# Kernel tuning notes

Measured on AMD Instinct MI355X. Metric: run time of the kernel, lower is better.

The kernel has to match this reference:

```python
import jax, jax.numpy as jnp
import numpy as np

N, E, G = 20000, 320000, 256
FXD, FXT, OD = 78, 954, 128


def _lin(key, fan_in, fan_out, scale=0.05):
    return jax.random.normal(key, (fan_in, fan_out), dtype=jnp.float32) * scale


def setup_inputs() -> dict:
    key = jax.random.key(0)
    ks = jax.random.split(key, 24)
    inp = {
        "x1": jax.random.normal(ks[0], (N, FXD), dtype=jnp.float32),
        "edge_index1": jax.random.randint(ks[1], (2, E), 0, N, dtype=jnp.int32),
        "batch1": (jnp.arange(N, dtype=jnp.int32) * G) // N,  # sorted, every graph non-empty
        "x2": jax.random.normal(ks[2], (N, FXD), dtype=jnp.float32),
        "edge_index2": jax.random.randint(ks[3], (2, E), 0, N, dtype=jnp.int32),
        "batch2": (jnp.arange(N, dtype=jnp.int32) * G) // N,
        "cell": jax.random.normal(ks[4], (G, FXT), dtype=jnp.float32),
        # GCNConv weights (shared across the two drug branches, as in the module)
        "Wc1": _lin(ks[5], FXD, FXD), "bc1": jnp.zeros((FXD,), jnp.float32),
        "Wc2": _lin(ks[6], FXD, FXD * 2), "bc2": jnp.zeros((FXD * 2,), jnp.float32),
        "Wc3": _lin(ks[7], FXD * 2, FXD * 4), "bc3": jnp.zeros((FXD * 4,), jnp.float32),
        "Wg1": _lin(ks[8], FXD * 4, FXD * 2), "bg1": jnp.zeros((FXD * 2,), jnp.float32),
        "Wg2": _lin(ks[9], FXD * 2, OD), "bg2": jnp.zeros((OD,), jnp.float32),
        # cell reduction MLP 954 -> 2048 -> 512 -> 256
        "Wr1": _lin(ks[10], FXT, 2048), "br1": jnp.zeros((2048,), jnp.float32),
        "Wr2": _lin(ks[11], 2048, 512), "br2": jnp.zeros((512,), jnp.float32),
        "Wr3": _lin(ks[12], 512, OD * 2), "br3": jnp.zeros((OD * 2,), jnp.float32),
        # head MLP 512 -> 1024 -> 512 -> 128 -> 2
        "Wf1": _lin(ks[13], OD * 4, 1024), "bf1": jnp.zeros((1024,), jnp.float32),
        "Wf2": _lin(ks[14], 1024, 512), "bf2": jnp.zeros((512,), jnp.float32),
        "Wf3": _lin(ks[15], 512, 128), "bf3": jnp.zeros((128,), jnp.float32),
        "Wo": _lin(ks[16], 128, 2), "bo": jnp.zeros((2,), jnp.float32),
    }
    return inp


def gcn_conv(x, W, b, src, dst, n):
    """PyG GCNConv: h = D^{-1/2}(A+I)D^{-1/2} (x W) + b (self-loops added)."""
    h = x @ W
    loops = jnp.arange(n, dtype=src.dtype)
    s = jnp.concatenate([src, loops])
    d = jnp.concatenate([dst, loops])
    deg = jax.ops.segment_sum(jnp.ones_like(s, dtype=h.dtype), d, num_segments=n)
    dinv = jax.lax.rsqrt(deg)  # deg >= 1 due to self-loops
    norm = dinv[s] * dinv[d]  # [E+N]
    out = jax.ops.segment_sum(h[s] * norm[:, None], d, num_segments=n)
    return out + b


def drug_branch(x, ei, batch, Wc1, bc1, Wc2, bc2, Wc3, bc3, Wg1, bg1, Wg2, bg2):
    src, dst = ei[0], ei[1]
    n = x.shape[0]
    x = jax.nn.relu(gcn_conv(x, Wc1, bc1, src, dst, n))
    x = jax.nn.relu(gcn_conv(x, Wc2, bc2, src, dst, n))
    x = jax.nn.relu(gcn_conv(x, Wc3, bc3, src, dst, n))
    x = jax.ops.segment_max(x, batch, num_segments=G)  # global max pool -> [G, 312]
    x = jax.nn.relu(x @ Wg1 + bg1)
    x = x @ Wg2 + bg2  # dropout is identity in eval mode
    return x


def reference(x1, edge_index1, batch1, x2, edge_index2, batch2, cell,
              Wc1, bc1, Wc2, bc2, Wc3, bc3, Wg1, bg1, Wg2, bg2,
              Wr1, br1, Wr2, br2, Wr3, br3,
              Wf1, bf1, Wf2, bf2, Wf3, bf3, Wo, bo):
    g1 = drug_branch(x1, edge_index1, batch1, Wc1, bc1, Wc2, bc2, Wc3, bc3, Wg1, bg1, Wg2, bg2)
    g2 = drug_branch(x2, edge_index2, batch2, Wc1, bc1, Wc2, bc2, Wc3, bc3, Wg1, bg1, Wg2, bg2)
    # F.normalize(cell, p=2, dim=1)
    cv = cell / jnp.maximum(jnp.linalg.norm(cell, axis=1, keepdims=True), 1e-12)
    cv = jax.nn.relu(cv @ Wr1 + br1)
    cv = jax.nn.relu(cv @ Wr2 + br2)
    cv = jax.nn.relu(cv @ Wr3 + br3)
    xc = jnp.concatenate([g1, g2, cv], axis=1)  # [G, 512]
    xc = jax.nn.relu(xc @ Wf1 + bf1)
    xc = jax.nn.relu(xc @ Wf2 + bf2)
    xc = jax.nn.relu(xc @ Wf3 + bf3)
    return xc @ Wo + bo  # [G, 2]
```

## Files before the change

### kernel.cpp

```cpp
#include <hip/hip_runtime.h>

#define N_NODES 20000
#define N_EDGES 320000
#define N_GRAPH 256
#define ECHUNK 2048

__device__ __forceinline__ ushort f2b(float f) {
  unsigned u = __float_as_uint(f);
  u += 0x7FFFu + ((u >> 16) & 1u);
  return (ushort)(u >> 16);
}
__device__ __forceinline__ float b2f(ushort u) {
  return __uint_as_float(((unsigned)u) << 16);
}

typedef __attribute__((ext_vector_type(8))) short bf16x8;
typedef __attribute__((ext_vector_type(4))) float f32x4;

template <int POOL>
__launch_bounds__(256)
__global__ void gemm_mfma(const ushort* __restrict__ A, int lda,
                          const ushort* __restrict__ Bt, int ldbt,
                          void* __restrict__ Cv, int ldc, int zstride,
                          const float* __restrict__ bias,
                          int Nr, int Kpad, int M, int do_relu, int obf,
                          int kchunk, int swz,
                          const int* __restrict__ bA, const int* __restrict__ bB,
                          int nsplit, int gA, int gB, int gTot) {
  constexpr int BM = 128, BN = 64, BK = 32, LK = 40;
  __shared__ __align__(16) ushort Asl[BM][LK];
  __shared__ __align__(16) ushort Bsl[BN][LK];
  const int tid = threadIdx.x;
  int bx, by;
  if (swz) {
    const int Cc = (M + BN - 1) / BN;
    const int R = (Nr + BM - 1) / BM;
    const int RR = (R + 7) >> 3;
    const int xz = blockIdx.x & 7, g = blockIdx.x >> 3;
    const int q = g / Cc;
    by = xz * RR + q;
    bx = g - q * Cc;
    if (by >= R) return;
  } else {
    bx = blockIdx.x; by = blockIdx.y;
  }
  const int row0 = by * BM, col0 = bx * BN;

  const int lane = tid & 63, w = tid >> 6;
  const int a_r = tid >> 1, a_h = tid & 1;
  const int b_r = tid >> 2, b_o = (tid & 3) * 8;

  const int klo = blockIdx.z * kchunk;
  const int khi = min(klo + kchunk, Kpad);
  const int nst = (khi - klo) / BK;

  uint4 pa0, pa1, pb0;
  auto load_tile = [&](int k0) {
    if (row0 + a_r < Nr) {
      const uint4* p = (const uint4*)(A + (size_t)(row0 + a_r) * lda + k0 + a_h * 16);
      pa0 = p[0]; pa1 = p[1];
    } else {
      pa0 = make_uint4(0u, 0u, 0u, 0u); pa1 = pa0;
    }
    pb0 = *(const uint4*)(Bt + (size_t)(col0 + b_r) * ldbt + k0 + b_o);
  };
  auto commit = [&]() {
    *(uint4*)&Asl[a_r][a_h * 16] = pa0;
    *(uint4*)&Asl[a_r][a_h * 16 + 8] = pa1;
    *(uint4*)&Bsl[b_r][b_o] = pb0;
  };

  f32x4 acc[2][4] = {};
  const int mrow = w * 32;
  const int lm = lane & 15, lq = (lane >> 4) * 8;

  load_tile(klo);
  for (int t = 0; t < nst; ++t) {
    commit();
    __syncthreads();
    if (t + 1 < nst) load_tile(klo + (t + 1) * BK);
    bf16x8 af0 = *(const bf16x8*)&Asl[mrow + lm][lq];
    bf16x8 af1 = *(const bf16x8*)&Asl[mrow + 16 + lm][lq];
    bf16x8 bf0 = *(const bf16x8*)&Bsl[lm][lq];
    bf16x8 bf1 = *(const bf16x8*)&Bsl[16 + lm][lq];
    bf16x8 bf2 = *(const bf16x8*)&Bsl[32 + lm][lq];
    bf16x8 bf3 = *(const bf16x8*)&Bsl[48 + lm][lq];
    acc[0][0] = __builtin_amdgcn_mfma_f32_16x16x32_bf16(af0, bf0, acc[0][0], 0, 0, 0);
    acc[0][1] = __builtin_amdgcn_mfma_f32_16x16x32_bf16(af0, bf1, acc[0][1], 0, 0, 0);
    acc[0][2] = __builtin_amdgcn_mfma_f32_16x16x32_bf16(af0, bf2, acc[0][2], 0, 0, 0);
    acc[0][3] = __builtin_amdgcn_mfma_f32_16x16x32_bf16(af0, bf3, acc[0][3], 0, 0, 0);
    acc[1][0] = __builtin_amdgcn_mfma_f32_16x16x32_bf16(af1, bf0, acc[1][0], 0, 0, 0);
    acc[1][1] = __builtin_amdgcn_mfma_f32_16x16x32_bf16(af1, bf1, acc[1][1], 0, 0, 0);
    acc[1][2] = __builtin_amdgcn_mfma_f32_16x16x32_bf16(af1, bf2, acc[1][2], 0, 0, 0);
    acc[1][3] = __builtin_amdgcn_mfma_f32_16x16x32_bf16(af1, bf3, acc[1][3], 0, 0, 0);
    __syncthreads();
  }

  const int rquad = (lane >> 4) * 4;

  if constexpr (POOL) {
    __shared__ int Ps[4][64];
    Ps[tid >> 6][tid & 63] = 0;
    __syncthreads();
    const int g0 = (row0 < nsplit) ? gA + bA[row0] : gB + bB[row0 - nsplit];
    int gr8[2][4];
#pragma unroll
    for (int mt = 0; mt < 2; ++mt)
#pragma unroll
      for (int r = 0; r < 4; ++r) {
        const int rr = row0 + mrow + mt * 16 + rquad + r;
        gr8[mt][r] = (rr < Nr)
                         ? ((rr < nsplit) ? gA + bA[rr] : gB + bB[rr - nsplit])
                         : -1;
      }
#pragma unroll
    for (int mt = 0; mt < 2; ++mt)
#pragma unroll
      for (int nt = 0; nt < 4; ++nt) {
        const int cl = nt * 16 + lm;
        if (col0 + cl >= M) continue;
        const float bv = bias[col0 + cl];
#pragma unroll
        for (int r = 0; r < 4; ++r) {
          const int g = gr8[mt][r];
          if (g < 0) continue;
          const float v = fmaxf(acc[mt][nt][r] + bv, 0.f);
          atomicMax(&Ps[g - g0][cl], __float_as_int(v));
        }
      }
    __syncthreads();
    const int s = tid >> 6, c = tid & 63;
    const int g = g0 + s, cc = col0 + c;
    if (g < gTot && cc < M)
      atomicMax((int*)Cv + (size_t)g * ldc + cc, Ps[s][c]);
    return;
  }

  if (zstride) {
    float* Cz = (float*)Cv + (size_t)blockIdx.z * zstride;
#pragma unroll
    for (int mt = 0; mt < 2; ++mt)
#pragma unroll
      for (int nt = 0; nt < 4; ++nt) {
        const int cc = col0 + nt * 16 + lm;
        if (cc >= M) continue;
#pragma unroll
        for (int r = 0; r < 4; ++r) {
          const int rr = row0 + mrow + mt * 16 + rquad + r;
          if (rr < Nr) Cz[(size_t)rr * ldc + cc] = acc[mt][nt][r];
        }
      }
    return;
  }
#pragma unroll
  for (int mt = 0; mt < 2; ++mt) {
#pragma unroll
    for (int nt = 0; nt < 4; ++nt) {
      const int cc = col0 + nt * 16 + lm;
      if (cc >= M) continue;
      const float bv = bias ? bias[cc] : 0.f;
#pragma unroll
      for (int r = 0; r < 4; ++r) {
        const int rr = row0 + mrow + mt * 16 + rquad + r;
        if (rr >= Nr) continue;
        float v = acc[mt][nt][r] + bv;
        if (do_relu) v = fmaxf(v, 0.f);
        if (obf) ((ushort*)Cv)[(size_t)rr * ldc + cc] = f2b(v);
        else     ((float*)Cv)[(size_t)rr * ldc + cc] = v;
      }
    }
  }
}

__global__ void wcvt_all(const float* __restrict__ W1, const float* __restrict__ W2,
                         const float* __restrict__ W3, const float* __restrict__ Wr1,
                         const float* __restrict__ Wr2, const float* __restrict__ Wf1,
                         ushort* __restrict__ T1, ushort* __restrict__ T2,
                         ushort* __restrict__ T3, ushort* __restrict__ R1,
                         ushort* __restrict__ R2, ushort* __restrict__ F1) {
  const int A1 = 128 * 96, A2 = A1 + 192 * 96, A3 = A2 + 320 * 160;
  const int S1 = 2048 * 960, S2 = 512 * 2048, S3 = 1024 * 512;
  int gid = blockIdx.x * blockDim.x + threadIdx.x;
  if (gid < A1) {
    int n = gid / 96, k = gid - n * 96;
    T1[gid] = (n < 78 && k < 78) ? f2b(W1[k * 78 + n]) : 0;
  } else if (gid < A2) {
    int g = gid - A1;
    int n = g / 96, k = g - n * 96;
    T2[g] = (n < 156 && k < 78) ? f2b(W2[k * 156 + n]) : 0;
  } else if (gid < A3) {
    int g = gid - A2;
    int n = g / 160, k = g - n * 160;
    T3[g] = (n < 312 && k < 156) ? f2b(W3[k * 312 + n]) : 0;
  } else if (gid < A3 + S1) {
    int g = gid - A3;
    int n = g / 960, k = g - n * 960;
    R1[g] = (k < 954) ? f2b(Wr1[(size_t)k * 2048 + n]) : 0;
  } else if (gid < A3 + S1 + S2) {
    int g = gid - A3 - S1;
    int n = g / 2048, k = g - n * 2048;
    R2[g] = f2b(Wr2[(size_t)k * 512 + n]);
  } else if (gid < A3 + S1 + S2 + S3) {
    int g = gid - A3 - S1 - S2;
    int n = g / 512, k = g - n * 512;
    F1[g] = f2b(Wf1[(size_t)k * 1024 + n]);
  }
}

template<int BM, int BN, int TM, int TN>
__launch_bounds__(256)
__global__ void gemm_t(const float* __restrict__ A, int lda,
                       const float* __restrict__ B, int ldb,
                       float* __restrict__ C, int ldc, int zstride,
                       const float* __restrict__ bias,
                       int Nr, int K, int M, int do_relu, int kchunk) {
  constexpr int BK = 16;
  constexpr int LDA = BM + 4;
  __shared__ __align__(16) float As[BK][LDA];
  __shared__ __align__(16) float Bs[BK][BN];
  const int tid = threadIdx.x;
  const int row0 = blockIdx.y * BM, col0 = blockIdx.x * BN;
  constexpr int NX = BN / TN;
  const int tx = tid % NX, ty = tid / NX;
  float acc[TM][TN] = {};
  const int klo = blockIdx.z * kchunk;
  const int khi = min(klo + kchunk, K);

  constexpr int AIT = BM * BK / 4 / 256;
  constexpr int BIT = BK * BN / 4 / 256;
  float4 pa[AIT], pb[BIT];

  auto load_tile = [&](int k0) {
#pragma unroll
    for (int it = 0; it < AIT; ++it) {
      const int s = it * 256 + tid;
      const int row = s >> 2, kq = (s & 3) << 2;
      float4 av = make_float4(0.f, 0.f, 0.f, 0.f);
      const int gr = row0 + row, gk = k0 + kq;
      if (gr < Nr) {
        const float* Ap = A + (size_t)gr * lda + gk;
        if (gk + 3 < khi) { av.x = Ap[0]; av.y = Ap[1]; av.z = Ap[2]; av.w = Ap[3]; }
        else {
          if (gk     < khi) av.x = Ap[0];
          if (gk + 1 < khi) av.y = Ap[1];
          if (gk + 2 < khi) av.z = Ap[2];
        }
      }
      pa[it] = av;
    }
#pragma unroll
    for (int it = 0; it < BIT; ++it) {
      const int s = it * 256 + tid;
      const int kr = s / (BN / 4), c = (s % (BN / 4)) << 2;
      float4 bv = make_float4(0.f, 0.f, 0.f, 0.f);
      const int gk = k0 + kr, gc = col0 + c;
      if (gk < khi) {
        const float* Bp = B + (size_t)gk * ldb + gc;
        if (gc + 3 < M) { bv.x = Bp[0]; bv.y = Bp[1]; bv.z = Bp[2]; bv.w = Bp[3]; }
        else {
          if (gc     < M) bv.x = Bp[0];
          if (gc + 1 < M) bv.y = Bp[1];
          if (gc + 2 < M) bv.z = Bp[2];
        }
      }
      pb[it] = bv;
    }
  };

  load_tile(klo);
  for (int k0 = klo; k0 < khi; k0 += BK) {
#pragma unroll
    for (int it = 0; it < AIT; ++it) {
      const int s = it * 256 + tid;
      const int row = s >> 2, kq = (s & 3) << 2;
      As[kq    ][row] = pa[it].x;
      As[kq + 1][row] = pa[it].y;
      As[kq + 2][row] = pa[it].z;
      As[kq + 3][row] = pa[it].w;
    }
#pragma unroll
    for (int it = 0; it < BIT; ++it) {
      const int s = it * 256 + tid;
      const int kr = s / (BN / 4), c = (s % (BN / 4)) << 2;
      *(float4*)&Bs[kr][c] = pb[it];
    }
    __syncthreads();
    if (k0 + BK < khi) load_tile(k0 + BK);
#pragma unroll
    for (int kk = 0; kk < BK; ++kk) {
      float ar[TM], br[TN];
#pragma unroll
      for (int i = 0; i < TM; i += 4)
        *(float4*)&ar[i] = *(const float4*)&As[kk][ty * TM + i];
      if constexpr (TN == 8) {
        *(float4*)&br[0] = *(const float4*)&Bs[kk][tx * 4];
        *(float4*)&br[4] = *(const float4*)&Bs[kk][BN / 2 + tx * 4];
      } else {
        *(float4*)&br[0] = *(const float4*)&Bs[kk][tx * TN];
      }
#pragma unroll
      for (int i = 0; i < TM; ++i)
#pragma unroll
        for (int j = 0; j < TN; ++j)
          acc[i][j] += ar[i] * br[j];
    }
    __syncthreads();
  }

  float* Cz = C + (size_t)blockIdx.z * zstride;
#pragma unroll
  for (int i = 0; i < TM; ++i) {
    const int r = row0 + ty * TM + i;
    if (r >= Nr) continue;
    float* Crow = Cz + (size_t)r * ldc;
#pragma unroll
    for (int g = 0; g < TN / 4; ++g) {
      const int c = col0 + (TN == 8 ? g * (BN / 2) : 0) + tx * 4;
      if (c + 3 < M) {
        float4 v;
        v.x = acc[i][g * 4 + 0]; v.y = acc[i][g * 4 + 1];
        v.z = acc[i][g * 4 + 2]; v.w = acc[i][g * 4 + 3];
        if (bias) { v.x += bias[c]; v.y += bias[c + 1]; v.z += bias[c + 2]; v.w += bias[c + 3]; }
        if (do_relu) {
          v.x = fmaxf(v.x, 0.f); v.y = fmaxf(v.y, 0.f);
          v.z = fmaxf(v.z, 0.f); v.w = fmaxf(v.w, 0.f);
        }
        *(float4*)&Crow[c] = v;
      } else {
#pragma unroll
        for (int j = 0; j < 4; ++j) {
          if (c + j >= M) continue;
          float v = acc[i][g * 4 + j];
          if (bias) v += bias[c + j];
          if (do_relu) v = fmaxf(v, 0.f);
          Crow[c + j] = v;
        }
      }
    }
  }
}

__global__ void bias_sum_kernel(const float* __restrict__ src, int zs, int Sz,
                                void* __restrict__ dstv, int ldd,
                                const float* __restrict__ bias,
                                int Nr, int M, int do_relu, int obf, int rsplit) {
  int idx = blockIdx.x * blockDim.x + threadIdx.x;
  if (idx >= Nr * M) return;
  int r = idx / M, c = idx - r * M;
  float v = bias[c];
  for (int z = 0; z < Sz; ++z) v += src[idx + (size_t)z * zs];
  if (do_relu) v = fmaxf(v, 0.f);
  int rm = r, rq = 0;
  if (rsplit) { rq = r / rsplit; rm = r - rq * rsplit; }
  size_t di = (size_t)rm * ldd + (size_t)rq * M + c;
  if (obf) ((ushort*)dstv)[di] = f2b(v);
  else     ((float*)dstv)[di] = v;
}

__global__ void histp_kernel(const int* __restrict__ e1, const int* __restrict__ e2,
                             int* __restrict__ cnt, int E, int npass, int rng) {
  const int xcd = blockIdx.x & 7;
  const int lo = xcd * rng, hi = lo + rng;
  const int base = (blockIdx.x >> 3) * ECHUNK;
  const int TE = npass * E;
  for (int i = threadIdx.x; i < ECHUNK; i += 256) {
    int e = base + i;
    if (e >= TE) break;
    int d = (e < E) ? e1[E + e] : N_NODES + e2[e - E + E];
    if (d >= lo && d < hi) atomicAdd(&cnt[d], 1);
  }
}

__global__ void scatterp_kernel(const int* __restrict__ e1, const int* __restrict__ e2,
                                int* __restrict__ cursor, ushort* __restrict__ col_idx,
                                int E, int npass, int rng) {
  const int xcd = blockIdx.x & 7;
  const int lo = xcd * rng, hi = lo + rng;
  const int base = (blockIdx.x >> 3) * ECHUNK;
  const int TE = npass * E;
  for (int i = threadIdx.x; i < ECHUNK; i += 256) {
    int e = base + i;
    if (e >= TE) break;
    int d, s;
    if (e < E) { d = e1[E + e]; s = e1[e]; }
    else { int j = e - E; d = N_NODES + e2[E + j]; s = N_NODES + e2[j]; }
    if (d >= lo && d < hi) {
      int p = atomicAdd(&cursor[d], 1);
      col_idx[p] = (ushort)s;
    }
  }
}

__launch_bounds__(1024)
__global__ void scan1_kernel(const int* __restrict__ cnt, int* __restrict__ row_ptr,
                             int* __restrict__ part, int n) {
  __shared__ int sh[1024];
  const int tid = threadIdx.x;
  const int i = blockIdx.x * 1024 + tid;
  const int v = (i < n) ? cnt[i] : 0;
  sh[tid] = v;
  __syncthreads();
#pragma unroll
  for (int off = 1; off < 1024; off <<= 1) {
    int t = (tid >= off) ? sh[tid - off] : 0;
    __syncthreads();
    sh[tid] += t;
    __syncthreads();
  }
  if (i < n) row_ptr[i] = sh[tid] - v;
  if (tid == 1023) part[blockIdx.x] = sh[tid];
}

__global__ void scan23_kernel(const int* __restrict__ cnt, int* __restrict__ row_ptr,
                              const int* __restrict__ part, int* __restrict__ cursor,
                              float* __restrict__ dinv, int n, int total,
                              const int* __restrict__ b1, const int* __restrict__ b2,
                              int* __restrict__ s1, int* __restrict__ s2) {
  __shared__ int base_sh;
  const int tid = threadIdx.x;
  if (tid == 0) {
    int blk = blockIdx.x >> 2;
    int s = 0;
    for (int b = 0; b < blk; ++b) s += part[b];
    base_sh = s;
  }
  __syncthreads();
  int i = blockIdx.x * 256 + tid;
  if (i >= n) return;
  int rp = row_ptr[i] + base_sh;
  row_ptr[i] = rp;
  cursor[i] = rp;
  dinv[i] = rsqrtf((float)(cnt[i] + 1));
  if (i == 0) row_ptr[n] = total;
  if (i < N_NODES) {
    if (i == 0) { s1[0] = 0; s1[N_GRAPH] = N_NODES; }
    else if (b1[i] != b1[i - 1]) s1[b1[i]] = i;
  } else {
    int j = i - N_NODES;
    if (j == 0) { s2[0] = N_NODES; s2[N_GRAPH] = 2 * N_NODES; }
    else if (b2[j] != b2[j - 1]) s2[b2[j]] = N_NODES + j;
  }
}

__global__ void tobf16_kernel(const float* __restrict__ xa, const float* __restrict__ xb,
                              int nsplit, ushort* __restrict__ dst, int total) {
  int gid = blockIdx.x * blockDim.x + threadIdx.x;
  if (gid >= total) return;
  int n = gid / 20, v = gid - n * 20;
  const float* src = (n < nsplit) ? xa + (size_t)n * 78 : xb + (size_t)(n - nsplit) * 78;
  int f0 = v * 4;
  ushort4 o;
  o.x = (f0     < 78) ? f2b(src[f0])     : 0;
  o.y = (f0 + 1 < 78) ? f2b(src[f0 + 1]) : 0;
  o.z = (f0 + 2 < 78) ? f2b(src[f0 + 2]) : 0;
  o.w = (f0 + 3 < 78) ? f2b(src[f0 + 3]) : 0;
  ((ushort4*)(dst + (size_t)n * 80))[v] = o;
}

__global__ void aggb_flat(const ushort* __restrict__ h, const int* __restrict__ row_ptr,
                          const ushort* __restrict__ col_idx, const float* __restrict__ dinv,
                          ushort* __restrict__ out, int in_ld, int out_ld,
                          int V, int total) {
  int gid = blockIdx.x * blockDim.x + threadIdx.x;
  if (gid >= total) return;
  int n = gid / V, v = gid - n * V;
  const float din = dinv[n];
  const ushort4* hv = (const ushort4*)h;
  const int ivs = in_ld >> 2;
  float4 a;
  {
    ushort4 u = hv[(size_t)n * ivs + v];
    a.x = din * b2f(u.x); a.y = din * b2f(u.y);
    a.z = din * b2f(u.z); a.w = din * b2f(u.w);
  }
  const int beg = row_ptr[n], end = row_ptr[n + 1];
  int e = beg;
  for (; e + 3 < end; e += 4) {
    int s0 = col_idx[e], s1 = col_idx[e + 1], s2 = col_idx[e + 2], s3 = col_idx[e + 3];
    float d0 = dinv[s0], d1 = dinv[s1], d2 = dinv[s2], d3 = dinv[s3];
    ushort4 u0 = hv[(size_t)s0 * ivs + v], u1 = hv[(size_t)s1 * ivs + v];
    ushort4 u2 = hv[(size_t)s2 * ivs + v], u3 = hv[(size_t)s3 * ivs + v];
    a.x += d0 * b2f(u0.x) + d1 * b2f(u1.x) + d2 * b2f(u2.x) + d3 * b2f(u3.x);
    a.y += d0 * b2f(u0.y) + d1 * b2f(u1.y) + d2 * b2f(u2.y) + d3 * b2f(u3.y);
    a.z += d0 * b2f(u0.z) + d1 * b2f(u1.z) + d2 * b2f(u2.z) + d3 * b2f(u3.z);
    a.w += d0 * b2f(u0.w) + d1 * b2f(u1.w) + d2 * b2f(u2.w) + d3 * b2f(u3.w);
  }
  for (; e < end; ++e) {
    int s0 = col_idx[e];
    float d0 = dinv[s0];
    ushort4 u0 = hv[(size_t)s0 * ivs + v];
    a.x += d0 * b2f(u0.x); a.y += d0 * b2f(u0.y);
    a.z += d0 * b2f(u0.z); a.w += d0 * b2f(u0.w);
  }
  ushort4 o;
  o.x = f2b(din * a.x); o.y = f2b(din * a.y);
  o.z = f2b(din * a.z); o.w = f2b(din * a.w);
  ((ushort4*)(out + (size_t)n * out_ld))[v] = o;
}

__global__ void rownorm_kernel(const float* __restrict__ cell, ushort* __restrict__ cv,
                               int F, int out_ld) {
  int g = blockIdx.x;
  __shared__ float red[256];
  int tid = threadIdx.x;
  const float* row = cell + (size_t)g * F;
  float s = 0.f;
  for (int f = tid; f < F; f += 256) { float v = row[f]; s += v * v; }
  red[tid] = s;
  __syncthreads();
  for (int off = 128; off > 0; off >>= 1) {
    if (tid < off) red[tid] += red[tid + off];
    __syncthreads();
  }
  float inv = 1.f / fmaxf(sqrtf(red[0]), 1e-12f);
  ushort* orow = cv + (size_t)g * out_ld;
  for (int f = tid; f < F; f += 256) orow[f] = f2b(row[f] * inv);
  for (int f = F + tid; f < out_ld; f += 256) orow[f] = 0;
}

extern "C" void kernel_launch(void* const* d_in, const int* in_sizes, int n_in,
                              void* d_out, int out_size, void* d_ws, size_t ws_size,
                              hipStream_t stream) {
  (void)in_sizes; (void)n_in; (void)out_size;
  const float* x1  = (const float*)d_in[0];
  const int*   ei1 = (const int*)d_in[1];
  const int*   bt1 = (const int*)d_in[2];
  const float* x2  = (const float*)d_in[3];
  const int*   ei2 = (const int*)d_in[4];
  const int*   bt2 = (const int*)d_in[5];
  const float* cell = (const float*)d_in[6];
  const float* Wc1 = (const float*)d_in[7];  const float* bc1 = (const float*)d_in[8];
  const float* Wc2 = (const float*)d_in[9];  const float* bc2 = (const float*)d_in[10];
  const float* Wc3 = (const float*)d_in[11]; const float* bc3 = (const float*)d_in[12];
  const float* Wg1 = (const float*)d_in[13]; const float* bg1 = (const float*)d_in[14];
  const float* Wg2 = (const float*)d_in[15]; const float* bg2 = (const float*)d_in[16];
  const float* Wr1 = (const float*)d_in[17]; const float* br1 = (const float*)d_in[18];
  const float* Wr2 = (const float*)d_in[19]; const float* br2 = (const float*)d_in[20];
  const float* Wr3 = (const float*)d_in[21]; const float* br3 = (const float*)d_in[22];
  const float* Wf1 = (const float*)d_in[23]; const float* bf1 = (const float*)d_in[24];
  const float* Wf2 = (const float*)d_in[25]; const float* bf2 = (const float*)d_in[26];
  const float* Wf3 = (const float*)d_in[27]; const float* bf3 = (const float*)d_in[28];
  const float* Wo  = (const float*)d_in[29]; const float* bo  = (const float*)d_in[30];
  float* out = (float*)d_out;

  const bool batched = ws_size >= (size_t)95 * 1024 * 1024;
  const int NPASS = batched ? 2 : 1;
  const int NN = NPASS * N_NODES;

  char* ws = (char*)d_ws;
  size_t off = 0;
  auto alloc_f = [&](size_t ne) { float* p = (float*)(ws + off); off += ne * 4; return p; };
  auto alloc_i = [&](size_t ne) { int* p = (int*)(ws + off); off += ne * 4; return p; };
  float* xbuf   = alloc_f((size_t)NN * 320);
  ushort* ab16  = (ushort*)alloc_f((size_t)NN * 80);
  ushort* xb16s = (ushort*)alloc_f((size_t)NN * 40);
  float* dinv   = alloc_f(NN);
  float* pooled = alloc_f((size_t)512 * 312);
  ushort* cv16  = (ushort*)alloc_f((size_t)N_GRAPH * 480);
  float* gtmp1  = alloc_f((size_t)512 * 2048);
  float* gtmp2  = alloc_f((size_t)512 * 512);
  float* gtmp3  = alloc_f((size_t)N_GRAPH * 256);
  ushort* catbuf = (ushort*)alloc_f((size_t)N_GRAPH * 256);
  ushort* gt1b  = (ushort*)alloc_f((size_t)N_GRAPH * 1024);
  ushort* wc1t  = (ushort*)alloc_f(128 * 96 / 2);
  ushort* wc2t  = (ushort*)alloc_f(192 * 96 / 2);
  ushort* wc3t  = (ushort*)alloc_f(320 * 160 / 2);
  ushort* wr1t  = (ushort*)alloc_f(2048 * 960 / 2);
  ushort* wr2t  = (ushort*)alloc_f(512 * 2048 / 2);
  ushort* wf1t  = (ushort*)alloc_f(1024 * 512 / 2);
  int* cnt     = alloc_i(NN);
  int* row_ptr = alloc_i(NN + 1);
  int* cursor  = alloc_i(NN);
  ushort* col_idx = (ushort*)alloc_i(NPASS * N_EDGES / 2);
  int* part    = alloc_i(64);
  int* start1  = alloc_i(N_GRAPH + 1);
  int* start2  = alloc_i(N_GRAPH + 1);
  float* accb  = xbuf;
  ushort* xb16w = (ushort*)xbuf;

  auto gemm_small = [&](const float* A, int lda, const float* B, int ldb, float* C, int ldc,
                        const float* bias, int Nr, int K, int M, int relu) {
    dim3 grid((M + 63) / 64, (Nr + 63) / 64, 1);
    gemm_t<64, 64, 4, 4><<<grid, 256, 0, stream>>>(A, lda, B, ldb, C, ldc, 0, bias,
                                                   Nr, K, M, relu, K);
  };
  auto splitk = [&](const float* A, int lda, const float* B, int M_, int K_, int S,
                    const float* bias, void* dst, int ldd, int relu, int Nr, int obf,
                    int rsplit) {
    int kchunk = (((K_ + S - 1) / S) + 15) / 16 * 16;
    int Sz = (K_ + kchunk - 1) / kchunk;
    dim3 grid((M_ + 63) / 64, (Nr + 63) / 64, Sz);
    gemm_t<64, 64, 4, 4><<<grid, 256, 0, stream>>>(A, lda, B, M_, accb, M_, Nr * M_,
                                                   nullptr, Nr, K_, M_, 0, kchunk);
    int tot = Nr * M_;
    bias_sum_kernel<<<(tot + 255) / 256, 256, 0, stream>>>(accb, Nr * M_, Sz, dst, ldd,
                                                           bias, Nr, M_, relu, obf, rsplit);
  };
  auto mfma = [&](const ushort* A, int lda, const ushort* Bt, int ldbt, void* C, int ldc,
                  const float* bias, int Nr, int Kpad, int M, int relu, int obf) {
    int Cc = (M + 63) / 64, R = (Nr + 127) / 128, RR = (R + 7) >> 3;
    dim3 grid(8 * RR * Cc, 1, 1);
    gemm_mfma<0><<<grid, 256, 0, stream>>>(A, lda, Bt, ldbt, C, ldc, 0, bias, Nr, Kpad, M,
                                           relu, obf, Kpad, 1,
                                           nullptr, nullptr, 0, 0, 0, 0);
  };
  auto mfma_pool = [&](const ushort* A, int lda, const ushort* Bt, int ldbt,
                       const float* bias, int Nr, int Kpad, int M,
                       const int* bA, const int* bB, int nsplit, int gA, int gB, int gTot) {
    int Cc = (M + 63) / 64, R = (Nr + 127) / 128, RR = (R + 7) >> 3;
    dim3 grid(8 * RR * Cc, 1, 1);
    gemm_mfma<1><<<grid, 256, 0, stream>>>(A, lda, Bt, ldbt, pooled, 312, 0, bias,
                                           Nr, Kpad, M, 1, 0, Kpad, 1,
                                           bA, bB, nsplit, gA, gB, gTot);
  };
  auto mfma_splitk = [&](const ushort* A, int lda, const ushort* Bt, int ldbt, int M_,
                         int Kpad, int kchunk, const float* bias, void* dst, int ldd,
                         int relu, int obf) {
    int Sz = (Kpad + kchunk - 1) / kchunk;
    dim3 grid((M_ + 63) / 64, 2, Sz);
    gemm_mfma<0><<<grid, 256, 0, stream>>>(A, lda, Bt, ldbt, accb, M_, N_GRAPH * M_, nullptr,
                                           N_GRAPH, Kpad, M_, 0, 0, kchunk, 0,
                                           nullptr, nullptr, 0, 0, 0, 0);
    int tot = N_GRAPH * M_;
    bias_sum_kernel<<<(tot + 255) / 256, 256, 0, stream>>>(accb, N_GRAPH * M_, Sz, dst, ldd,
                                                           bias, N_GRAPH, M_, relu, obf, 0);
  };

  {
    int tot = 128 * 96 + 192 * 96 + 320 * 160 + 2048 * 960 + 512 * 2048 + 1024 * 512;
    wcvt_all<<<(tot + 255) / 256, 256, 0, stream>>>(Wc1, Wc2, Wc3, Wr1, Wr2, Wf1,
                                                    wc1t, wc2t, wc3t, wr1t, wr2t, wf1t);
  }
  hipMemsetAsync(pooled, 0, (size_t)2 * N_GRAPH * 312 * sizeof(float), stream);

  auto drug_pass = [&](const float* xa, const float* xb, const int* eia, const int* eib,
                       const int* bta, const int* btb, int npass, int pool_base) {
    const int nn = npass * N_NODES;
    const int te = npass * N_EDGES;
    const int nb = (nn + 1023) / 1024;
    const int rng = nn / 8;
    const int echunks = (te + ECHUNK - 1) / ECHUNK;
    hipMemsetAsync(cnt, 0, nn * sizeof(int), stream);
    histp_kernel<<<8 * echunks, 256, 0, stream>>>(eia, eib, cnt, N_EDGES, npass, rng);
    scan1_kernel<<<nb, 1024, 0, stream>>>(cnt, row_ptr, part, nn);
    scan23_kernel<<<(nn + 255) / 256, 256, 0, stream>>>(cnt, row_ptr, part, cursor, dinv,
                                                        nn, te, bta, btb, start1, start2);
    scatterp_kernel<<<8 * echunks, 256, 0, stream>>>(eia, eib, cursor, col_idx,
                                                     N_EDGES, npass, rng);
    {
      int tot = nn * 20;
      tobf16_kernel<<<(tot + 255) / 256, 256, 0, stream>>>(
          xa, xb, (npass == 2) ? N_NODES : nn, xb16s, tot);
    }
    {
      int tot = nn * 20;
      aggb_flat<<<(tot + 255) / 256, 256, 0, stream>>>(xb16s, row_ptr, col_idx, dinv,
                                                       ab16, 80, 96, 20, tot);
    }
    mfma(ab16, 96, wc1t, 96, xb16s, 80, bc1, nn, 96, 78, 1, 1);
    {
      int tot = nn * 20;
      aggb_flat<<<(tot + 255) / 256, 256, 0, stream>>>(xb16s, row_ptr, col_idx, dinv,
                                                       ab16, 80, 96, 20, tot);
    }
    mfma(ab16, 96, wc2t, 96, xb16w, 160, bc2, nn, 96, 156, 1, 1);
    {
      int tot = nn * 40;
      aggb_flat<<<(tot + 255) / 256, 256, 0, stream>>>(xb16w, row_ptr, col_idx, dinv,
                                                       ab16, 160, 160, 40, tot);
    }
    mfma_pool(ab16, 160, wc3t, 160, bc3, nn, 160, 312,
              bta, btb, (npass == 2) ? N_NODES : nn,
              pool_base, pool_base + N_GRAPH, pool_base + npass * N_GRAPH);
  };

  if (batched) {
    drug_pass(x1, x2, ei1, ei2, bt1, bt2, 2, 0);
  } else {
    drug_pass(x1, x1, ei1, ei1, bt1, bt1, 1, 0);
    drug_pass(x2, x2, ei2, ei2, bt2, bt2, 1, N_GRAPH);
  }

  splitk(pooled, 312, Wg1, 156, 312, 4, bg1, gtmp1, 156, 1, 2 * N_GRAPH, 0, 0);
  splitk(gtmp1, 156, Wg2, 128, 156, 2, bg2, catbuf, 512, 0, 2 * N_GRAPH, 1, 256);

  rownorm_kernel<<<N_GRAPH, 256, 0, stream>>>(cell, cv16, 954, 960);
  mfma_splitk(cv16, 960, wr1t, 960, 2048, 960, 256, br1, gt1b, 2048, 1, 1);
  mfma_splitk(gt1b, 2048, wr2t, 2048, 512, 2048, 256, br2, gtmp2, 512, 1, 0);
  splitk(gtmp2, 512, Wr3, 256, 512, 16, br3, catbuf + 256, 512, 1, N_GRAPH, 1, 0);
  mfma_splitk(catbuf, 512, wf1t, 512, 1024, 512, 128, bf1, gtmp1, 1024, 1, 0);
  splitk(gtmp1, 1024, Wf2, 512, 1024, 32, bf2, gtmp2, 512, 1, N_GRAPH, 0, 0);
  splitk(gtmp2, 512, Wf3, 128, 512, 32, bf3, gtmp3, 128, 1, N_GRAPH, 0, 0);
  gemm_small(gtmp3, 128, Wo, 2, out, 2, bo, N_GRAPH, 128, 2, 0);
}
```

Before: 436.0 us.

## Replace split-K tail GEMMs with grouped in-block MFMA kernel and merge launches

Replaces the fp32 split-K GEMMs and their separate bias/sum kernels for the pooled-graph MLP, cell MLP and head MLP with a single grouped bf16 MFMA kernel. Each block reduces K across its four waves in shared memory and applies bias, ReLU and the bf16 store in one pass. Independent GEMMs from the drug and cell branches are paired into one launch. Weight conversion and cell row normalization are merged into one prep kernel, the edge scatter is fused with the x->bf16 conversion, and the pooled-buffer zeroing is folded into the existing memset. The aim is fewer launches and no split-K partial round trips. In exchange, bf16 precision now also covers the Wg, Wr3, Wf2 and Wf3 layers.

```diff
diff --git a/kernel.cpp b/kernel.cpp
--- a/kernel.cpp
+++ b/kernel.cpp
@@ -172,39 +172,171 @@
   }
 }
 
-__global__ void wcvt_all(const float* __restrict__ W1, const float* __restrict__ W2,
-                         const float* __restrict__ W3, const float* __restrict__ Wr1,
-                         const float* __restrict__ Wr2, const float* __restrict__ Wf1,
-                         ushort* __restrict__ T1, ushort* __restrict__ T2,
-                         ushort* __restrict__ T3, ushort* __restrict__ R1,
-                         ushort* __restrict__ R2, ushort* __restrict__ F1) {
-  const int A1 = 128 * 96, A2 = A1 + 192 * 96, A3 = A2 + 320 * 160;
-  const int S1 = 2048 * 960, S2 = 512 * 2048, S3 = 1024 * 512;
-  int gid = blockIdx.x * blockDim.x + threadIdx.x;
-  if (gid < A1) {
-    int n = gid / 96, k = gid - n * 96;
-    T1[gid] = (n < 78 && k < 78) ? f2b(W1[k * 78 + n]) : 0;
-  } else if (gid < A2) {
-    int g = gid - A1;
-    int n = g / 96, k = g - n * 96;
-    T2[g] = (n < 156 && k < 78) ? f2b(W2[k * 156 + n]) : 0;
-  } else if (gid < A3) {
-    int g = gid - A2;
-    int n = g / 160, k = g - n * 160;
-    T3[g] = (n < 312 && k < 156) ? f2b(W3[k * 312 + n]) : 0;
-  } else if (gid < A3 + S1) {
-    int g = gid - A3;
-    int n = g / 960, k = g - n * 960;
-    R1[g] = (k < 954) ? f2b(Wr1[(size_t)k * 2048 + n]) : 0;
-  } else if (gid < A3 + S1 + S2) {
-    int g = gid - A3 - S1;
-    int n = g / 2048, k = g - n * 2048;
-    R2[g] = f2b(Wr2[(size_t)k * 512 + n]);
-  } else if (gid < A3 + S1 + S2 + S3) {
-    int g = gid - A3 - S1 - S2;
-    int n = g / 512, k = g - n * 512;
-    F1[g] = f2b(Wf1[(size_t)k * 1024 + n]);
-  }
+struct GJob {
+  const void* A; const ushort* Bt; void* C; const float* bias;
+  int lda, a_f32, ldbt, ldc, Nr, Kpad, M, relu, obf, rsplit, cpad, rb, cb, blk0;
+};
+
+__launch_bounds__(256)
+__global__ void gemm_grp(GJob j0, GJob j1, int njobs) {
+  GJob j = (njobs > 1 && (int)blockIdx.x >= j1.blk0) ? j1 : j0;
+  const int local = blockIdx.x - j.blk0;
+  const int by = local / j.cb, bx = local - by * j.cb;
+  const int row0 = by * 32, col0 = bx * 64;
+  const int tid = threadIdx.x, lane = tid & 63, w = tid >> 6;
+
+  __shared__ __align__(16) char smem[32768];
+  ushort (*Asl)[32][40] = (ushort (*)[32][40])smem;
+  ushort (*Bsl)[64][40] = (ushort (*)[64][40])(smem + 10240);
+  float  (*Rs)[32][64]  = (float  (*)[32][64])smem;
+
+  const int a_r = lane >> 1, a_h = lane & 1;
+  const int lm = lane & 15, lq = (lane >> 4) * 8;
+  const int nst = j.Kpad / 32;
+
+  uint4 ra[4], rb[4];
+  auto gload = [&](int t) {
+    const int k0 = t * 32;
+    const int ar = row0 + a_r;
+    if (j.a_f32) {
+      if (ar < j.Nr) {
+        const uint4* p = (const uint4*)((const float*)j.A + (size_t)ar * j.lda + k0 + a_h * 16);
+        ra[0] = p[0]; ra[1] = p[1]; ra[2] = p[2]; ra[3] = p[3];
+      } else {
+        ra[0] = make_uint4(0u, 0u, 0u, 0u); ra[1] = ra[0]; ra[2] = ra[0]; ra[3] = ra[0];
+      }
+    } else {
+      if (ar < j.Nr) {
+        const uint4* p = (const uint4*)((const ushort*)j.A + (size_t)ar * j.lda + k0 + a_h * 16);
+        ra[0] = p[0]; ra[1] = p[1];
+      } else {
+        ra[0] = make_uint4(0u, 0u, 0u, 0u); ra[1] = ra[0];
+      }
+    }
+    const uint4* q = (const uint4*)(j.Bt + (size_t)(col0 + lane) * j.ldbt + k0);
+    rb[0] = q[0]; rb[1] = q[1]; rb[2] = q[2]; rb[3] = q[3];
+  };
+  auto commit = [&]() {
+    if (j.a_f32) {
+      ushort tmp[16];
+      const float* f = (const float*)&ra[0];
+#pragma unroll
+      for (int q2 = 0; q2 < 16; ++q2) tmp[q2] = f2b(f[q2]);
+      *(uint4*)&Asl[w][a_r][a_h * 16]     = *(uint4*)&tmp[0];
+      *(uint4*)&Asl[w][a_r][a_h * 16 + 8] = *(uint4*)&tmp[8];
+    } else {
+      *(uint4*)&Asl[w][a_r][a_h * 16]     = ra[0];
+      *(uint4*)&Asl[w][a_r][a_h * 16 + 8] = ra[1];
+    }
+    *(uint4*)&Bsl[w][lane][0]  = rb[0];
+    *(uint4*)&Bsl[w][lane][8]  = rb[1];
+    *(uint4*)&Bsl[w][lane][16] = rb[2];
+    *(uint4*)&Bsl[w][lane][24] = rb[3];
+  };
+
+  f32x4 acc[2][4] = {};
+  if (w < nst) {
+    gload(w);
+    for (int t = w; t < nst; t += 4) {
+      commit();
+      bf16x8 af0 = *(const bf16x8*)&Asl[w][lm][lq];
+      bf16x8 af1 = *(const bf16x8*)&Asl[w][16 + lm][lq];
+      bf16x8 bq0 = *(const bf16x8*)&Bsl[w][lm][lq];
+      bf16x8 bq1 = *(const bf16x8*)&Bsl[w][16 + lm][lq];
+      bf16x8 bq2 = *(const bf16x8*)&Bsl[w][32 + lm][lq];
+      bf16x8 bq3 = *(const bf16x8*)&Bsl[w][48 + lm][lq];
+      if (t + 4 < nst) gload(t + 4);
+      acc[0][0] = __builtin_amdgcn_mfma_f32_16x16x32_bf16(af0, bq0, acc[0][0], 0, 0, 0);
+      acc[0][1] = __builtin_amdgcn_mfma_f32_16x16x32_bf16(af0, bq1, acc[0][1], 0, 0, 0);
+      acc[0][2] = __builtin_amdgcn_mfma_f32_16x16x32_bf16(af0, bq2, acc[0][2], 0, 0, 0);
+      acc[0][3] = __builtin_amdgcn_mfma_f32_16x16x32_bf16(af0, bq3, acc[0][3], 0, 0, 0);
+      acc[1][0] = __builtin_amdgcn_mfma_f32_16x16x32_bf16(af1, bq0, acc[1][0], 0, 0, 0);
+      acc[1][1] = __builtin_amdgcn_mfma_f32_16x16x32_bf16(af1, bq1, acc[1][1], 0, 0, 0);
+      acc[1][2] = __builtin_amdgcn_mfma_f32_16x16x32_bf16(af1, bq2, acc[1][2], 0, 0, 0);
+      acc[1][3] = __builtin_amdgcn_mfma_f32_16x16x32_bf16(af1, bq3, acc[1][3], 0, 0, 0);
+    }
+  }
+
+  __syncthreads();
+  const int rquad = (lane >> 4) * 4;
+#pragma unroll
+  for (int mt = 0; mt < 2; ++mt)
+#pragma unroll
+    for (int nt = 0; nt < 4; ++nt)
+#pragma unroll
+      for (int r = 0; r < 4; ++r)
+        Rs[w][mt * 16 + rquad + r][nt * 16 + lm] = acc[mt][nt][r];
+  __syncthreads();
+
+  const int rrow = tid >> 3, cs = (tid & 7) * 8;
+  float v[8];
+  {
+    float4 x0 = *(const float4*)&Rs[0][rrow][cs];
+    float4 x1 = *(const float4*)&Rs[0][rrow][cs + 4];
+    v[0] = x0.x; v[1] = x0.y; v[2] = x0.z; v[3] = x0.w;
+    v[4] = x1.x; v[5] = x1.y; v[6] = x1.z; v[7] = x1.w;
+  }
+#pragma unroll
+  for (int ww = 1; ww < 4; ++ww) {
+    float4 x0 = *(const float4*)&Rs[ww][rrow][cs];
+    float4 x1 = *(const float4*)&Rs[ww][rrow][cs + 4];
+    v[0] += x0.x; v[1] += x0.y; v[2] += x0.z; v[3] += x0.w;
+    v[4] += x1.x; v[5] += x1.y; v[6] += x1.z; v[7] += x1.w;
+  }
+  const int rg = row0 + rrow;
+  if (rg < j.Nr) {
+    int rm = rg, rq = 0;
+    if (j.rsplit) { rq = rg / j.rsplit; rm = rg - rq * j.rsplit; }
+#pragma unroll
+    for (int q = 0; q < 8; ++q) {
+      const int cc = col0 + cs + q;
+      if (cc >= j.cpad) break;
+      float x = 0.f;
+      if (cc < j.M) {
+        x = v[q] + j.bias[cc];
+        if (j.relu) x = fmaxf(x, 0.f);
+      }
+      const size_t di = (size_t)rm * j.ldc + (size_t)rq * j.M + cc;
+      if (j.obf) ((ushort*)j.C)[di] = f2b(x);
+      else       ((float*)j.C)[di] = x;
+    }
+  }
+}
+
+struct WJob { const float* W; ushort* T; int Mv, Kv, Mp, Kp, blk0; };
+struct WArgs { WJob j[11]; int wblocks; const float* cell; ushort* cv; };
+
+__launch_bounds__(256)
+__global__ void prep_all(WArgs a) {
+  __shared__ float red[256];
+  const int bid = blockIdx.x, tid = threadIdx.x;
+  if (bid < a.wblocks) {
+    int ji = 0;
+#pragma unroll
+    for (int i = 1; i < 11; ++i)
+      if (bid >= a.j[i].blk0) ji = i;
+    WJob wj = a.j[ji];
+    int el = (bid - wj.blk0) * 256 + tid;
+    if (el < wj.Mp * wj.Kp) {
+      int n = el / wj.Kp, k = el - n * wj.Kp;
+      wj.T[el] = (n < wj.Mv && k < wj.Kv) ? f2b(wj.W[(size_t)k * wj.Mv + n]) : 0;
+    }
+    return;
+  }
+  const int g = bid - a.wblocks;
+  const float* row = a.cell + (size_t)g * 954;
+  float s = 0.f;
+  for (int f = tid; f < 954; f += 256) { float vv = row[f]; s += vv * vv; }
+  red[tid] = s;
+  __syncthreads();
+  for (int off2 = 128; off2 > 0; off2 >>= 1) {
+    if (tid < off2) red[tid] += red[tid + off2];
+    __syncthreads();
+  }
+  const float inv = 1.f / fmaxf(sqrtf(red[0]), 1e-12f);
+  ushort* orow = a.cv + (size_t)g * 960;
+  for (int f = tid; f < 954; f += 256) orow[f] = f2b(row[f] * inv);
+  for (int f = 954 + tid; f < 960; f += 256) orow[f] = 0;
 }
 
 template<int BM, int BN, int TM, int TN>
@@ -340,23 +472,6 @@
   }
 }
 
-__global__ void bias_sum_kernel(const float* __restrict__ src, int zs, int Sz,
-                                void* __restrict__ dstv, int ldd,
-                                const float* __restrict__ bias,
-                                int Nr, int M, int do_relu, int obf, int rsplit) {
-  int idx = blockIdx.x * blockDim.x + threadIdx.x;
-  if (idx >= Nr * M) return;
-  int r = idx / M, c = idx - r * M;
-  float v = bias[c];
-  for (int z = 0; z < Sz; ++z) v += src[idx + (size_t)z * zs];
-  if (do_relu) v = fmaxf(v, 0.f);
-  int rm = r, rq = 0;
-  if (rsplit) { rq = r / rsplit; rm = r - rq * rsplit; }
-  size_t di = (size_t)rm * ldd + (size_t)rq * M + c;
-  if (obf) ((ushort*)dstv)[di] = f2b(v);
-  else     ((float*)dstv)[di] = v;
-}
-
 __global__ void histp_kernel(const int* __restrict__ e1, const int* __restrict__ e2,
                              int* __restrict__ cnt, int E, int npass, int rng) {
   const int xcd = blockIdx.x & 7;
@@ -371,24 +486,40 @@
   }
 }
 
-__global__ void scatterp_kernel(const int* __restrict__ e1, const int* __restrict__ e2,
+__global__ void scat_cvt_kernel(const int* __restrict__ e1, const int* __restrict__ e2,
                                 int* __restrict__ cursor, ushort* __restrict__ col_idx,
-                                int E, int npass, int rng) {
-  const int xcd = blockIdx.x & 7;
-  const int lo = xcd * rng, hi = lo + rng;
-  const int base = (blockIdx.x >> 3) * ECHUNK;
-  const int TE = npass * E;
-  for (int i = threadIdx.x; i < ECHUNK; i += 256) {
-    int e = base + i;
-    if (e >= TE) break;
-    int d, s;
-    if (e < E) { d = e1[E + e]; s = e1[e]; }
-    else { int j = e - E; d = N_NODES + e2[E + j]; s = N_NODES + e2[j]; }
-    if (d >= lo && d < hi) {
-      int p = atomicAdd(&cursor[d], 1);
-      col_idx[p] = (ushort)s;
-    }
-  }
+                                int E, int npass, int rng, int scat_blocks,
+                                const float* __restrict__ xa, const float* __restrict__ xb,
+                                int nsplit, ushort* __restrict__ dst, int total16) {
+  if ((int)blockIdx.x < scat_blocks) {
+    const int xcd = blockIdx.x & 7;
+    const int lo = xcd * rng, hi = lo + rng;
+    const int base = (blockIdx.x >> 3) * ECHUNK;
+    const int TE = npass * E;
+    for (int i = threadIdx.x; i < ECHUNK; i += 256) {
+      int e = base + i;
+      if (e >= TE) break;
+      int d, s;
+      if (e < E) { d = e1[E + e]; s = e1[e]; }
+      else { int jj = e - E; d = N_NODES + e2[E + jj]; s = N_NODES + e2[jj]; }
+      if (d >= lo && d < hi) {
+        int p = atomicAdd(&cursor[d], 1);
+        col_idx[p] = (ushort)s;
+      }
+    }
+    return;
+  }
+  int gid = (blockIdx.x - scat_blocks) * 256 + threadIdx.x;
+  if (gid >= total16) return;
+  int n = gid / 20, v = gid - n * 20;
+  const float* src = (n < nsplit) ? xa + (size_t)n * 78 : xb + (size_t)(n - nsplit) * 78;
+  int f0 = v * 4;
+  ushort4 o;
+  o.x = (f0     < 78) ? f2b(src[f0])     : 0;
+  o.y = (f0 + 1 < 78) ? f2b(src[f0 + 1]) : 0;
+  o.z = (f0 + 2 < 78) ? f2b(src[f0 + 2]) : 0;
+  o.w = (f0 + 3 < 78) ? f2b(src[f0 + 3]) : 0;
+  ((ushort4*)(dst + (size_t)n * 80))[v] = o;
 }
 
 __launch_bounds__(1024)
@@ -442,21 +573,6 @@
   }
 }
 
-__global__ void tobf16_kernel(const float* __restrict__ xa, const float* __restrict__ xb,
-                              int nsplit, ushort* __restrict__ dst, int total) {
-  int gid = blockIdx.x * blockDim.x + threadIdx.x;
-  if (gid >= total) return;
-  int n = gid / 20, v = gid - n * 20;
-  const float* src = (n < nsplit) ? xa + (size_t)n * 78 : xb + (size_t)(n - nsplit) * 78;
-  int f0 = v * 4;
-  ushort4 o;
-  o.x = (f0     < 78) ? f2b(src[f0])     : 0;
-  o.y = (f0 + 1 < 78) ? f2b(src[f0 + 1]) : 0;
-  o.z = (f0 + 2 < 78) ? f2b(src[f0 + 2]) : 0;
-  o.w = (f0 + 3 < 78) ? f2b(src[f0 + 3]) : 0;
-  ((ushort4*)(dst + (size_t)n * 80))[v] = o;
-}
-
 __global__ void aggb_flat(const ushort* __restrict__ h, const int* __restrict__ row_ptr,
                           const ushort* __restrict__ col_idx, const float* __restrict__ dinv,
                           ushort* __restrict__ out, int in_ld, int out_ld,
@@ -496,26 +612,6 @@
   o.x = f2b(din * a.x); o.y = f2b(din * a.y);
   o.z = f2b(din * a.z); o.w = f2b(din * a.w);
   ((ushort4*)(out + (size_t)n * out_ld))[v] = o;
-}
-
-__global__ void rownorm_kernel(const float* __restrict__ cell, ushort* __restrict__ cv,
-                               int F, int out_ld) {
-  int g = blockIdx.x;
-  __shared__ float red[256];
-  int tid = threadIdx.x;
-  const float* row = cell + (size_t)g * F;
-  float s = 0.f;
-  for (int f = tid; f < F; f += 256) { float v = row[f]; s += v * v; }
-  red[tid] = s;
-  __syncthreads();
-  for (int off = 128; off > 0; off >>= 1) {
-    if (tid < off) red[tid] += red[tid + off];
-    __syncthreads();
-  }
-  float inv = 1.f / fmaxf(sqrtf(red[0]), 1e-12f);
-  ushort* orow = cv + (size_t)g * out_ld;
-  for (int f = tid; f < F; f += 256) orow[f] = f2b(row[f] * inv);
-  for (int f = F + tid; f < out_ld; f += 256) orow[f] = 0;
 }
 
 extern "C" void kernel_launch(void* const* d_in, const int* in_sizes, int n_in,
@@ -549,52 +645,51 @@
 
   char* ws = (char*)d_ws;
   size_t off = 0;
-  auto alloc_f = [&](size_t ne) { float* p = (float*)(ws + off); off += ne * 4; return p; };
-  auto alloc_i = [&](size_t ne) { int* p = (int*)(ws + off); off += ne * 4; return p; };
-  float* xbuf   = alloc_f((size_t)NN * 320);
+  auto alloc_f = [&](size_t ne) {
+    ne = (ne + 3) & ~(size_t)3;
+    float* p = (float*)(ws + off); off += ne * 4; return p;
+  };
+  auto alloc_i = [&](size_t ne) {
+    ne = (ne + 3) & ~(size_t)3;
+    int* p = (int*)(ws + off); off += ne * 4; return p;
+  };
+  ushort* xb16w = (ushort*)alloc_f((size_t)NN * 80);
   ushort* ab16  = (ushort*)alloc_f((size_t)NN * 80);
   ushort* xb16s = (ushort*)alloc_f((size_t)NN * 40);
   float* dinv   = alloc_f(NN);
-  float* pooled = alloc_f((size_t)512 * 312);
+  int* cnt      = alloc_i(NN);
+  float* pooled = alloc_f((size_t)512 * 320);
   ushort* cv16  = (ushort*)alloc_f((size_t)N_GRAPH * 480);
-  float* gtmp1  = alloc_f((size_t)512 * 2048);
-  float* gtmp2  = alloc_f((size_t)512 * 512);
-  float* gtmp3  = alloc_f((size_t)N_GRAPH * 256);
-  ushort* catbuf = (ushort*)alloc_f((size_t)N_GRAPH * 256);
-  ushort* gt1b  = (ushort*)alloc_f((size_t)N_GRAPH * 1024);
+  ushort* wg1o  = (ushort*)alloc_f((size_t)512 * 80);
+  ushort* wr1o  = (ushort*)alloc_f((size_t)256 * 1024);
+  ushort* wr2o  = (ushort*)alloc_f((size_t)256 * 256);
+  ushort* catbuf = (ushort*)alloc_f((size_t)256 * 256);
+  ushort* wf1o  = (ushort*)alloc_f((size_t)256 * 512);
+  ushort* wf2o  = (ushort*)alloc_f((size_t)256 * 256);
+  float* wf3o   = alloc_f((size_t)256 * 128);
   ushort* wc1t  = (ushort*)alloc_f(128 * 96 / 2);
   ushort* wc2t  = (ushort*)alloc_f(192 * 96 / 2);
   ushort* wc3t  = (ushort*)alloc_f(320 * 160 / 2);
   ushort* wr1t  = (ushort*)alloc_f(2048 * 960 / 2);
   ushort* wr2t  = (ushort*)alloc_f(512 * 2048 / 2);
   ushort* wf1t  = (ushort*)alloc_f(1024 * 512 / 2);
-  int* cnt     = alloc_i(NN);
-  int* row_ptr = alloc_i(NN + 1);
+  ushort* wg1t  = (ushort*)alloc_f(192 * 320 / 2);
+  ushort* wg2t  = (ushort*)alloc_f(128 * 160 / 2);
+  ushort* wr3t  = (ushort*)alloc_f(256 * 512 / 2);
+  ushort* wf2t  = (ushort*)alloc_f(512 * 1024 / 2);
+  ushort* wf3t  = (ushort*)alloc_f(128 * 512 / 2);
+  int* row_ptr = alloc_i(NN + 4);
   int* cursor  = alloc_i(NN);
   ushort* col_idx = (ushort*)alloc_i(NPASS * N_EDGES / 2);
   int* part    = alloc_i(64);
-  int* start1  = alloc_i(N_GRAPH + 1);
-  int* start2  = alloc_i(N_GRAPH + 1);
-  float* accb  = xbuf;
-  ushort* xb16w = (ushort*)xbuf;
+  int* start1  = alloc_i(N_GRAPH + 4);
+  int* start2  = alloc_i(N_GRAPH + 4);
 
   auto gemm_small = [&](const float* A, int lda, const float* B, int ldb, float* C, int ldc,
                         const float* bias, int Nr, int K, int M, int relu) {
     dim3 grid((M + 63) / 64, (Nr + 63) / 64, 1);
     gemm_t<64, 64, 4, 4><<<grid, 256, 0, stream>>>(A, lda, B, ldb, C, ldc, 0, bias,
                                                    Nr, K, M, relu, K);
-  };
-  auto splitk = [&](const float* A, int lda, const float* B, int M_, int K_, int S,
-                    const float* bias, void* dst, int ldd, int relu, int Nr, int obf,
-                    int rsplit) {
-    int kchunk = (((K_ + S - 1) / S) + 15) / 16 * 16;
-    int Sz = (K_ + kchunk - 1) / kchunk;
-    dim3 grid((M_ + 63) / 64, (Nr + 63) / 64, Sz);
-    gemm_t<64, 64, 4, 4><<<grid, 256, 0, stream>>>(A, lda, B, M_, accb, M_, Nr * M_,
-                                                   nullptr, Nr, K_, M_, 0, kchunk);
-    int tot = Nr * M_;
-    bias_sum_kernel<<<(tot + 255) / 256, 256, 0, stream>>>(accb, Nr * M_, Sz, dst, ldd,
-                                                           bias, Nr, M_, relu, obf, rsplit);
   };
   auto mfma = [&](const ushort* A, int lda, const ushort* Bt, int ldbt, void* C, int ldc,
                   const float* bias, int Nr, int Kpad, int M, int relu, int obf) {
@@ -609,48 +704,70 @@
                        const int* bA, const int* bB, int nsplit, int gA, int gB, int gTot) {
     int Cc = (M + 63) / 64, R = (Nr + 127) / 128, RR = (R + 7) >> 3;
     dim3 grid(8 * RR * Cc, 1, 1);
-    gemm_mfma<1><<<grid, 256, 0, stream>>>(A, lda, Bt, ldbt, pooled, 312, 0, bias,
+    gemm_mfma<1><<<grid, 256, 0, stream>>>(A, lda, Bt, ldbt, pooled, 320, 0, bias,
                                            Nr, Kpad, M, 1, 0, Kpad, 1,
                                            bA, bB, nsplit, gA, gB, gTot);
   };
-  auto mfma_splitk = [&](const ushort* A, int lda, const ushort* Bt, int ldbt, int M_,
-                         int Kpad, int kchunk, const float* bias, void* dst, int ldd,
-                         int relu, int obf) {
-    int Sz = (Kpad + kchunk - 1) / kchunk;
-    dim3 grid((M_ + 63) / 64, 2, Sz);
-    gemm_mfma<0><<<grid, 256, 0, stream>>>(A, lda, Bt, ldbt, accb, M_, N_GRAPH * M_, nullptr,
-                                           N_GRAPH, Kpad, M_, 0, 0, kchunk, 0,
-                                           nullptr, nullptr, 0, 0, 0, 0);
-    int tot = N_GRAPH * M_;
-    bias_sum_kernel<<<(tot + 255) / 256, 256, 0, stream>>>(accb, N_GRAPH * M_, Sz, dst, ldd,
-                                                           bias, N_GRAPH, M_, relu, obf, 0);
+  auto mkjob = [&](const void* A, int lda, int a_f32, const ushort* Bt, int ldbt,
+                   void* C, int ldc, const float* bias, int Nr, int Kpad, int M,
+                   int relu, int obf, int rsplit, int cpad) {
+    GJob g; g.A = A; g.Bt = Bt; g.C = C; g.bias = bias;
+    g.lda = lda; g.a_f32 = a_f32; g.ldbt = ldbt; g.ldc = ldc;
+    g.Nr = Nr; g.Kpad = Kpad; g.M = M; g.relu = relu; g.obf = obf;
+    g.rsplit = rsplit; g.cpad = cpad;
+    g.rb = (Nr + 31) / 32; g.cb = (M + 63) / 64; g.blk0 = 0;
+    return g;
+  };
+  auto grp1 = [&](GJob a) {
+    gemm_grp<<<a.rb * a.cb, 256, 0, stream>>>(a, a, 1);
+  };
+  auto grp2 = [&](GJob a, GJob b) {
+    b.blk0 = a.rb * a.cb;
+    gemm_grp<<<b.blk0 + b.rb * b.cb, 256, 0, stream>>>(a, b, 2);
   };
 
   {
-    int tot = 128 * 96 + 192 * 96 + 320 * 160 + 2048 * 960 + 512 * 2048 + 1024 * 512;
-    wcvt_all<<<(tot + 255) / 256, 256, 0, stream>>>(Wc1, Wc2, Wc3, Wr1, Wr2, Wf1,
-                                                    wc1t, wc2t, wc3t, wr1t, wr2t, wf1t);
-  }
-  hipMemsetAsync(pooled, 0, (size_t)2 * N_GRAPH * 312 * sizeof(float), stream);
+    WArgs wa{};
+    int nj = 0, wb = 0;
+    auto addw = [&](const float* W, ushort* T, int Mv, int Kv, int Mp, int Kp) {
+      wa.j[nj].W = W; wa.j[nj].T = T; wa.j[nj].Mv = Mv; wa.j[nj].Kv = Kv;
+      wa.j[nj].Mp = Mp; wa.j[nj].Kp = Kp; wa.j[nj].blk0 = wb;
+      wb += (Mp * Kp + 255) / 256; ++nj;
+    };
+    addw(Wc1, wc1t,   78,   78,  128,   96);
+    addw(Wc2, wc2t,  156,   78,  192,   96);
+    addw(Wc3, wc3t,  312,  156,  320,  160);
+    addw(Wr1, wr1t, 2048,  954, 2048,  960);
+    addw(Wr2, wr2t,  512, 2048,  512, 2048);
+    addw(Wf1, wf1t, 1024,  512, 1024,  512);
+    addw(Wg1, wg1t,  156,  312,  192,  320);
+    addw(Wg2, wg2t,  128,  156,  128,  160);
+    addw(Wr3, wr3t,  256,  512,  256,  512);
+    addw(Wf2, wf2t,  512, 1024,  512, 1024);
+    addw(Wf3, wf3t,  128,  512,  128,  512);
+    wa.wblocks = wb; wa.cell = cell; wa.cv = cv16;
+    prep_all<<<wb + N_GRAPH, 256, 0, stream>>>(wa);
+  }
 
   auto drug_pass = [&](const float* xa, const float* xb, const int* eia, const int* eib,
-                       const int* bta, const int* btb, int npass, int pool_base) {
+                       const int* bta, const int* btb, int npass, int pool_base,
+                       int zero_pool) {
     const int nn = npass * N_NODES;
     const int te = npass * N_EDGES;
     const int nb = (nn + 1023) / 1024;
     const int rng = nn / 8;
     const int echunks = (te + ECHUNK - 1) / ECHUNK;
-    hipMemsetAsync(cnt, 0, nn * sizeof(int), stream);
+    hipMemsetAsync(cnt, 0, (size_t)nn * 4 + (zero_pool ? (size_t)512 * 320 * 4 : 0),
+                   stream);
     histp_kernel<<<8 * echunks, 256, 0, stream>>>(eia, eib, cnt, N_EDGES, npass, rng);
     scan1_kernel<<<nb, 1024, 0, stream>>>(cnt, row_ptr, part, nn);
     scan23_kernel<<<(nn + 255) / 256, 256, 0, stream>>>(cnt, row_ptr, part, cursor, dinv,
                                                         nn, te, bta, btb, start1, start2);
-    scatterp_kernel<<<8 * echunks, 256, 0, stream>>>(eia, eib, cursor, col_idx,
-                                                     N_EDGES, npass, rng);
     {
-      int tot = nn * 20;
-      tobf16_kernel<<<(tot + 255) / 256, 256, 0, stream>>>(
-          xa, xb, (npass == 2) ? N_NODES : nn, xb16s, tot);
+      int nb16 = (nn * 20 + 255) / 256;
+      scat_cvt_kernel<<<8 * echunks + nb16, 256, 0, stream>>>(
+          eia, eib, cursor, col_idx, N_EDGES, npass, rng, 8 * echunks,
+          xa, xb, (npass == 2) ? N_NODES : nn, xb16s, nn * 20);
     }
     {
       int tot = nn * 20;
@@ -675,21 +792,19 @@
   };
 
   if (batched) {
-    drug_pass(x1, x2, ei1, ei2, bt1, bt2, 2, 0);
+    drug_pass(x1, x2, ei1, ei2, bt1, bt2, 2, 0, 1);
   } else {
-    drug_pass(x1, x1, ei1, ei1, bt1, bt1, 1, 0);
-    drug_pass(x2, x2, ei2, ei2, bt2, bt2, 1, N_GRAPH);
-  }
-
-  splitk(pooled, 312, Wg1, 156, 312, 4, bg1, gtmp1, 156, 1, 2 * N_GRAPH, 0, 0);
-  splitk(gtmp1, 156, Wg2, 128, 156, 2, bg2, catbuf, 512, 0, 2 * N_GRAPH, 1, 256);
-
-  rownorm_kernel<<<N_GRAPH, 256, 0, stream>>>(cell, cv16, 954, 960);
-  mfma_splitk(cv16, 960, wr1t, 960, 2048, 960, 256, br1, gt1b, 2048, 1, 1);
-  mfma_splitk(gt1b, 2048, wr2t, 2048, 512, 2048, 256, br2, gtmp2, 512, 1, 0);
-  splitk(gtmp2, 512, Wr3, 256, 512, 16, br3, catbuf + 256, 512, 1, N_GRAPH, 1, 0);
-  mfma_splitk(catbuf, 512, wf1t, 512, 1024, 512, 128, bf1, gtmp1, 1024, 1, 0);
-  splitk(gtmp1, 1024, Wf2, 512, 1024, 32, bf2, gtmp2, 512, 1, N_GRAPH, 0, 0);
-  splitk(gtmp2, 512, Wf3, 128, 512, 32, bf3, gtmp3, 128, 1, N_GRAPH, 0, 0);
-  gemm_small(gtmp3, 128, Wo, 2, out, 2, bo, N_GRAPH, 128, 2, 0);
-}
+    drug_pass(x1, x1, ei1, ei1, bt1, bt1, 1, 0, 1);
+    drug_pass(x2, x2, ei2, ei2, bt2, bt2, 1, N_GRAPH, 0);
+  }
+
+  grp2(mkjob(pooled, 320, 1, wg1t, 320, wg1o, 160, bg1, 512, 320, 156, 1, 1, 0, 160),
+       mkjob(cv16,   960, 0, wr1t, 960, wr1o, 2048, br1, 256, 960, 2048, 1, 1, 0, 2048));
+  grp2(mkjob(wg1o,  160, 0, wg2t,  160, catbuf, 512, bg2, 512,  160,  128, 0, 1, 256, 128),
+       mkjob(wr1o, 2048, 0, wr2t, 2048, wr2o,   512, br2, 256, 2048,  512, 1, 1, 0, 512));
+  grp1(mkjob(wr2o, 512, 0, wr3t, 512, catbuf + 256, 512, br3, 256, 512, 256, 1, 1, 0, 256));
+  grp1(mkjob(catbuf, 512, 0, wf1t,  512, wf1o, 1024, bf1, 256,  512, 1024, 1, 1, 0, 1024));
+  grp1(mkjob(wf1o,  1024, 0, wf2t, 1024, wf2o,  512, bf2, 256, 1024,  512, 1, 1, 0, 512));
+  grp1(mkjob(wf2o,   512, 0, wf3t,  512, wf3o,  128, bf3, 256,  512,  128, 1, 0, 0, 128));
+  gemm_small(wf3o, 128, Wo, 2, out, 2, bo, N_GRAPH, 128, 2, 0);
+}
```

Result: no change. 430.5 us (-1.3%).
